# Optimization experiments

Measured on AMD Instinct MI355X. Metric: run time of the kernel, lower is better.

## Reference

```python
import jax, jax.numpy as jnp
import numpy as np
import math

D_MODEL = 1024
NUM_HEADS = 16
HEAD = D_MODEL // NUM_HEADS
EPS = 1e-5


def setup_inputs() -> dict:
    key = jax.random.key(0)
    ks = jax.random.split(key, 5)
    x = jax.random.normal(ks[0], (2, 2048, D_MODEL), dtype=jnp.float32)
    # parameters (torch.rand -> uniform [0,1) per the module; scaled here for numerics)
    wq = jax.random.uniform(ks[1], (NUM_HEADS, D_MODEL, HEAD), dtype=jnp.float32) * 0.02
    wk = jax.random.uniform(ks[2], (NUM_HEADS, D_MODEL, HEAD), dtype=jnp.float32) * 0.02
    wv = jax.random.uniform(ks[3], (NUM_HEADS, D_MODEL, HEAD), dtype=jnp.float32) * 0.02
    wo = jax.random.uniform(ks[4], (D_MODEL, D_MODEL), dtype=jnp.float32) * 0.02
    ln_w = jnp.ones((D_MODEL,), dtype=jnp.float32)
    ln_b = jnp.zeros((D_MODEL,), dtype=jnp.float32)
    return {"x": x, "ln_w": ln_w, "ln_b": ln_b, "wq": wq, "wk": wk, "wv": wv, "wo": wo}


def _layernorm(x, w, b):
    mean = jnp.mean(x, axis=-1, keepdims=True)
    var = jnp.var(x, axis=-1, keepdims=True)
    return (x - mean) * w / jnp.sqrt(var + EPS) + b


def reference(x, ln_w, ln_b, wq, wk, wv, wo):
    # pre-norm
    y = _layernorm(x, ln_w, ln_b)  # [b, s, d]
    seq_len = y.shape[-2]
    # per-head projections: [b, h, s, e]
    q = jnp.einsum('bsd,hde->bhse', y, wq)
    k = jnp.einsum('bsd,hde->bhse', y, wk)
    v = jnp.einsum('bsd,hde->bhse', y, wv)
    scores = jnp.einsum('bhse,bhte->bhst', q, k) / math.sqrt(HEAD)
    causal = jnp.triu(jnp.full((seq_len, seq_len), -jnp.inf, dtype=scores.dtype), k=1)
    scores = scores + causal
    weights = jax.nn.softmax(scores, axis=-1)
    attn = jnp.einsum('bhst,bhte->bshe', weights, v)  # merged transpose
    attn = attn.reshape(*attn.shape[:-2], -1)  # [b, s, d]
    out = attn @ wo
    return out + x
```

## Files before the change

### kernel.cpp

```cpp
#include <hip/hip_runtime.h>
#include <stdint.h>

typedef __bf16 bf16;
typedef __bf16 bf16x2 __attribute__((ext_vector_type(2)));
typedef __bf16 bf16x4 __attribute__((ext_vector_type(4)));
typedef __bf16 bf16x8 __attribute__((ext_vector_type(8)));
typedef float f32x4 __attribute__((ext_vector_type(4)));
typedef unsigned int u32;
typedef u32 u32x4 __attribute__((ext_vector_type(4)));

#define D_MODEL 1024
#define NHEADS 16
#define HEADDIM 64
#define SEQ 2048
#define NBATCH 2

__device__ __forceinline__ void async_load16(const void* g, void* l) {
  __builtin_amdgcn_global_load_lds(
      (__attribute__((address_space(1))) void*)g,
      (__attribute__((address_space(3))) void*)l, 16, 0, 0);
}

__device__ __forceinline__ float fexp2(float x) {
#if __has_builtin(__builtin_amdgcn_exp2f)
  return __builtin_amdgcn_exp2f(x);
#else
  return exp2f(x);
#endif
}

__device__ __forceinline__ void pswap32(u32& x, u32& y) {
  asm("v_permlane32_swap_b32 %0, %1" : "+v"(x), "+v"(y));
}
__device__ __forceinline__ void pswap16(u32& x, u32& y) {
  asm("v_permlane16_swap_b32 %0, %1" : "+v"(x), "+v"(y));
}

__global__ __launch_bounds__(256)
void ln_and_transpose(const float* __restrict__ x, const float* __restrict__ lw,
                      const float* __restrict__ lb, bf16* __restrict__ y,
                      const float* __restrict__ wq, const float* __restrict__ wk,
                      const float* __restrict__ wv, const float* __restrict__ wo,
                      bf16* __restrict__ WqkvT, bf16* __restrict__ woT) {
  __shared__ float tile[64][65];
  __shared__ float ps[4], pq[4];
  int t = threadIdx.x;
  if (blockIdx.x < 4096) {
    int row = blockIdx.x;
    const float4 v = ((const float4*)(x + (size_t)row * D_MODEL))[t];
    float s = v.x + v.y + v.z + v.w;
    float sq = v.x * v.x + v.y * v.y + v.z * v.z + v.w * v.w;
#pragma unroll
    for (int d = 1; d < 64; d <<= 1) {
      s += __shfl_xor(s, d);
      sq += __shfl_xor(sq, d);
    }
    if ((t & 63) == 0) { ps[t >> 6] = s; pq[t >> 6] = sq; }
    __syncthreads();
    s = ps[0] + ps[1] + ps[2] + ps[3];
    sq = pq[0] + pq[1] + pq[2] + pq[3];
    float mean = s * (1.0f / D_MODEL);
    float var = sq * (1.0f / D_MODEL) - mean * mean;
    float rstd = rsqrtf(var + 1e-5f);
    float4 wv4 = ((const float4*)lw)[t];
    float4 bv = ((const float4*)lb)[t];
    bf16x4 o;
    o[0] = (bf16)((v.x - mean) * rstd * wv4.x + bv.x);
    o[1] = (bf16)((v.y - mean) * rstd * wv4.y + bv.y);
    o[2] = (bf16)((v.z - mean) * rstd * wv4.z + bv.z);
    o[3] = (bf16)((v.w - mean) * rstd * wv4.w + bv.w);
    ((bf16x4*)(y + (size_t)row * D_MODEL))[t] = o;
    return;
  }
  int blk = blockIdx.x - 4096;
  const float* s;
  bf16* d;
  int src_ld, dst_ld;
  if (blk < 768) {
    int wsel = blk >> 8;
    int rem = blk & 255;
    int h = rem >> 4, tr = rem & 15;
    const float* w3 = (wsel == 0) ? wq : (wsel == 1) ? wk : wv;
    s = w3 + (size_t)h * 65536 + (size_t)tr * 64 * 64;
    d = WqkvT + ((size_t)wsel << 20) + (size_t)h * 65536 + (size_t)tr * 64;
    src_ld = 64; dst_ld = 1024;
  } else {
    int r = blk - 768;
    int tr = r >> 4, tc = r & 15;
    s = wo + (size_t)(tr * 64) * 1024 + tc * 64;
    d = woT + (size_t)(tc * 64) * 1024 + tr * 64;
    src_ld = 1024; dst_ld = 1024;
  }
  int rr = t >> 4;
  int cc = (t & 15) << 2;
#pragma unroll
  for (int i = 0; i < 4; ++i) {
    float4 v = *(const float4*)&s[(size_t)(rr + i * 16) * src_ld + cc];
    tile[rr + i * 16][cc + 0] = v.x;
    tile[rr + i * 16][cc + 1] = v.y;
    tile[rr + i * 16][cc + 2] = v.z;
    tile[rr + i * 16][cc + 3] = v.w;
  }
  __syncthreads();
#pragma unroll
  for (int i = 0; i < 4; ++i) {
    int drow = rr + i * 16;
    bf16x4 o;
    o[0] = (bf16)tile[cc + 0][drow];
    o[1] = (bf16)tile[cc + 1][drow];
    o[2] = (bf16)tile[cc + 2][drow];
    o[3] = (bf16)tile[cc + 3][drow];
    *(bf16x4*)&d[(size_t)drow * dst_ld + cc] = o;
  }
}

template <int MODE, int BM, int BN>
__global__ __launch_bounds__(256)
void gemm_bt(const bf16* __restrict__ A, const bf16* __restrict__ Bt,
             int ntn, void* __restrict__ p0, void* __restrict__ p1,
             void* __restrict__ p2) {
  constexpr int NWR = BM / 64;
  constexpr int NWC = 4 / NWR;
  constexpr int NJ = BN / (16 * NWC);
  __shared__ __align__(16) bf16 As[2][BM * 64];
  __shared__ __align__(16) bf16 Bs[2][BN * 64];
  int cpx = gridDim.x >> 3;
  int wg = (blockIdx.x & 7) * cpx + (blockIdx.x >> 3);
  int bm = wg / ntn;
  int bn = wg % ntn;
  int t = threadIdx.x;
  int w = t >> 6, l = t & 63;
  int lg = l >> 4, lo = l & 15;
  int wr = w / NWC, wc = w % NWC;
  const bf16* Ab = A + (size_t)bm * BM * 1024;
  const bf16* Bb = Bt + (size_t)bn * BN * 1024;
  f32x4 acc[4][NJ];
#pragma unroll
  for (int i = 0; i < 4; ++i)
#pragma unroll
    for (int j = 0; j < NJ; ++j) acc[i][j] = (f32x4){0.f, 0.f, 0.f, 0.f};

  auto stage = [&](int bufi, int k0) {
#pragma unroll
    for (int it = 0; it < BM / 32; ++it) {
      int flat = it * 2048 + t * 8;
      int row = flat >> 6, sc = ((flat & 63) >> 3) ^ (row & 7);
      async_load16(Ab + (size_t)row * 1024 + k0 + sc * 8, &As[bufi][it * 2048 + w * 512]);
    }
#pragma unroll
    for (int it = 0; it < BN / 32; ++it) {
      int flat = it * 2048 + t * 8;
      int row = flat >> 6, sc = ((flat & 63) >> 3) ^ (row & 7);
      async_load16(Bb + (size_t)row * 1024 + k0 + sc * 8, &Bs[bufi][it * 2048 + w * 512]);
    }
  };

  stage(0, 0);
  __syncthreads();
  int buf = 0;
  for (int k0 = 0; k0 < 1024; k0 += 64) {
    if (k0 + 64 < 1024) stage(buf ^ 1, k0 + 64);
#pragma unroll
    for (int kk = 0; kk < 2; ++kk) {
      bf16x8 af[4], bfr[NJ];
#pragma unroll
      for (int i = 0; i < 4; ++i) {
        int row = wr * 64 + i * 16 + lo;
        af[i] = *(const bf16x8*)&As[buf][row * 64 + (((4 * kk + lg) ^ (lo & 7)) * 8)];
      }
#pragma unroll
      for (int j = 0; j < NJ; ++j) {
        int row = wc * (NJ * 16) + j * 16 + lo;
        bfr[j] = *(const bf16x8*)&Bs[buf][row * 64 + (((4 * kk + lg) ^ (lo & 7)) * 8)];
      }
#pragma unroll
      for (int i = 0; i < 4; ++i)
#pragma unroll
        for (int j = 0; j < NJ; ++j)
          acc[i][j] = __builtin_amdgcn_mfma_f32_16x16x32_bf16(af[i], bfr[j], acc[i][j], 0, 0, 0);
    }
    __syncthreads();
    buf ^= 1;
  }

  int mbase = bm * BM + wr * 64;
  int nbase = bn * BN + wc * (NJ * 16);
#pragma unroll
  for (int i = 0; i < 4; ++i) {
#pragma unroll
    for (int j = 0; j < NJ; ++j) {
      int row0 = mbase + i * 16 + lg * 4;
      int col = nbase + j * 16 + lo;
      if (MODE == 0) {
        if (col < 2048) {
          bf16* dst = (bf16*)(col < 1024 ? p0 : p1);
          int c = col & 1023;
          int h = c >> 6, e = c & 63;
#pragma unroll
          for (int r = 0; r < 4; ++r) {
            int row = row0 + r;
            dst[((((size_t)(row >> 11) * NHEADS + h) * SEQ) + (row & 2047)) * HEADDIM + e] =
                (bf16)acc[i][j][r];
          }
        } else {
          int c = col - 2048;
          int h = c >> 6, e = c & 63;
          int b_ = row0 >> 11, s_ = row0 & 2047;
          bf16x4 pk;
          pk[0] = (bf16)acc[i][j][0]; pk[1] = (bf16)acc[i][j][1];
          pk[2] = (bf16)acc[i][j][2]; pk[3] = (bf16)acc[i][j][3];
          *(bf16x4*)&((bf16*)p2)[(((size_t)b_ * NHEADS + h) * HEADDIM + e) * SEQ + s_] = pk;
        }
      } else {
#pragma unroll
        for (int r = 0; r < 4; ++r) {
          int row = row0 + r;
          float xr = ((const float*)p1)[(size_t)row * 1024 + col];
          ((float*)p0)[(size_t)row * 1024 + col] = acc[i][j][r] + xr;
        }
      }
    }
  }
}

__global__ __launch_bounds__(512)
void attn_kernel(const bf16* __restrict__ q, const bf16* __restrict__ k,
                 const bf16* __restrict__ vt, bf16* __restrict__ attn,
                 bf16* __restrict__ pO, float* __restrict__ plsum) {
  __shared__ __align__(16) bf16 Ks[2][64 * 64];
  __shared__ __align__(16) bf16 Vs[2][64 * 64];
  const float C2 = 0.125f * 1.44269504f;
  const float MC = 128.0f * C2;
  int i = blockIdx.x;
  int slot = i >> 3;
  int bh = (i & 7) + 8 * (slot & 3);
  int ji = slot >> 2;
  int split, tb;
  if (ji < 8) { split = 0; tb = ji; }
  else { split = 1 + ((ji >> 4) & 1); tb = 15 - (ji & 7); }
  int c0 = (split == 2) ? tb + 1 : 0;
  int c1 = (split == 1) ? tb + 1 : 2 * tb + 2;
  int b = bh >> 4, h = bh & 15;
  int t = threadIdx.x, w = t >> 6, l = t & 63;
  int lg = l >> 4, lo = l & 15;
  const bf16* qp = q + (size_t)bh * SEQ * HEADDIM;
  const bf16* kp = k + (size_t)bh * SEQ * HEADDIM;
  const bf16* vp = vt + (size_t)bh * HEADDIM * SEQ;
  int q0 = tb * 128 + w * 16;
  int cd = q0 >> 6;
  int diag_rhs = (w & 3) * 16 + lo;

  bf16x8 qf0 = *(const bf16x8*)&qp[(size_t)(q0 + lo) * HEADDIM + 8 * lg];
  bf16x8 qf1 = *(const bf16x8*)&qp[(size_t)(q0 + lo) * HEADDIM + 32 + 8 * lg];

  auto stage = [&](int bufi, int kv0) {
    int row = t >> 3, c16 = t & 7;
    int sc = c16 ^ (row & 7);
    async_load16(kp + (size_t)(kv0 + row) * HEADDIM + sc * 8, &Ks[bufi][t * 8]);
    async_load16(vp + (size_t)row * SEQ + kv0 + sc * 8, &Vs[bufi][t * 8]);
  };

  f32x4 o[4];
#pragma unroll
  for (int nt = 0; nt < 4; ++nt) o[nt] = (f32x4){0.f, 0.f, 0.f, 0.f};
  float lsum = 0.f;

  int buf = 0;
  stage(0, c0 * 64);
  __syncthreads();

  for (int c = c0; c < c1; ++c) {
    if (c + 1 < c1) stage(buf ^ 1, (c + 1) * 64);

    if (c <= cd) {
      f32x4 s[4];
      __builtin_amdgcn_s_setprio(1);
#pragma unroll
      for (int nt = 0; nt < 4; ++nt) {
        s[nt] = (f32x4){0.f, 0.f, 0.f, 0.f};
        int krow = nt * 16 + lo;
        bf16x8 kf0 = *(const bf16x8*)&Ks[buf][krow * 64 + ((lg ^ (lo & 7)) * 8)];
        bf16x8 kf1 = *(const bf16x8*)&Ks[buf][krow * 64 + (((4 + lg) ^ (lo & 7)) * 8)];
        s[nt] = __builtin_amdgcn_mfma_f32_16x16x32_bf16(kf0, qf0, s[nt], 0, 0, 0);
        s[nt] = __builtin_amdgcn_mfma_f32_16x16x32_bf16(kf1, qf1, s[nt], 0, 0, 0);
      }
      __builtin_amdgcn_s_setprio(0);

      bf16x8 vf0[4], vf1[4];
#pragma unroll
      for (int nt = 0; nt < 4; ++nt) {
        int vrow = nt * 16 + lo;
        vf0[nt] = *(const bf16x8*)&Vs[buf][vrow * 64 + ((lg ^ (lo & 7)) * 8)];
        vf1[nt] = *(const bf16x8*)&Vs[buf][vrow * 64 + (((4 + lg) ^ (lo & 7)) * 8)];
      }

      if (c == cd) {
#pragma unroll
        for (int nt = 0; nt < 4; ++nt)
#pragma unroll
          for (int r = 0; r < 4; ++r)
            s[nt][r] = (16 * nt + 4 * lg + r <= diag_rhs) ? s[nt][r] : -1e30f;
      }

      u32 W[4][2];
      float psum = 0.f;
#pragma unroll
      for (int nt = 0; nt < 4; ++nt) {
        float e0 = fexp2(fmaf(s[nt][0], C2, -MC));
        float e1 = fexp2(fmaf(s[nt][1], C2, -MC));
        float e2 = fexp2(fmaf(s[nt][2], C2, -MC));
        float e3 = fexp2(fmaf(s[nt][3], C2, -MC));
        psum += (e0 + e1) + (e2 + e3);
        bf16x2 w0, w1;
        w0[0] = (bf16)e0; w0[1] = (bf16)e1;
        w1[0] = (bf16)e2; w1[1] = (bf16)e3;
        W[nt][0] = __builtin_bit_cast(u32, w0);
        W[nt][1] = __builtin_bit_cast(u32, w1);
      }
      psum += __shfl_xor(psum, 16);
      psum += __shfl_xor(psum, 32);
      lsum += psum;

      u32 t0 = W[0][0], t2 = W[1][0];
      pswap32(t0, t2); pswap16(t0, t2);
      u32 t1 = W[0][1], t3 = W[1][1];
      pswap32(t1, t3); pswap16(t1, t3);
      u32 u0 = W[2][0], u2 = W[3][0];
      pswap32(u0, u2); pswap16(u0, u2);
      u32 u1 = W[2][1], u3 = W[3][1];
      pswap32(u1, u3); pswap16(u1, u3);
      u32x4 pw0 = {t0, t1, t2, t3};
      u32x4 pw1 = {u0, u1, u2, u3};
      bf16x8 pf0 = __builtin_bit_cast(bf16x8, pw0);
      bf16x8 pf1 = __builtin_bit_cast(bf16x8, pw1);

      __builtin_amdgcn_s_setprio(1);
#pragma unroll
      for (int nt = 0; nt < 4; ++nt) {
        o[nt] = __builtin_amdgcn_mfma_f32_16x16x32_bf16(pf0, vf0[nt], o[nt], 0, 0, 0);
        o[nt] = __builtin_amdgcn_mfma_f32_16x16x32_bf16(pf1, vf1[nt], o[nt], 0, 0, 0);
      }
      __builtin_amdgcn_s_setprio(0);
    }

    __syncthreads();
    buf ^= 1;
  }

  if (split == 0) {
#pragma unroll
    for (int r = 0; r < 4; ++r) {
      float ls = __shfl(lsum, (l & 48) | (4 * lg + r));
      float inv = 1.0f / ls;
      int qrow = q0 + 4 * lg + r;
#pragma unroll
      for (int nt = 0; nt < 4; ++nt)
        attn[((size_t)b * SEQ + qrow) * D_MODEL + h * HEADDIM + nt * 16 + lo] =
            (bf16)(o[nt][r] * inv);
    }
  } else {
    int half = split - 1;
#pragma unroll
    for (int r = 0; r < 4; ++r) {
      float ls = __shfl(lsum, (l & 48) | (4 * lg + r));
      int prow = q0 - 1024 + 4 * lg + r;
      if (lo == 0) plsum[(half << 15) + (bh << 10) + prow] = ls;
      size_t base = (((size_t)half * 32 + bh) * 1024 + prow) * 64;
#pragma unroll
      for (int nt = 0; nt < 4; ++nt)
        pO[base + nt * 16 + lo] = (bf16)o[nt][r];
    }
  }
}

__global__ __launch_bounds__(256)
void merge_kernel(const bf16* __restrict__ pO, const float* __restrict__ plsum,
                  bf16* __restrict__ attn) {
  int tid = blockIdx.x * 256 + threadIdx.x;
  int bh = tid >> 13;
  int rem = tid & 8191;
  int srow = rem >> 3, q8 = rem & 7;
  int b = bh >> 4, h = bh & 15;
  float l = plsum[(bh << 10) + srow] + plsum[(1 << 15) + (bh << 10) + srow];
  float inv = 1.0f / l;
  size_t base = (((size_t)bh) * 1024 + srow) * 64 + q8 * 8;
  bf16x8 a1 = *(const bf16x8*)&pO[base];
  bf16x8 a2 = *(const bf16x8*)&pO[(size_t)32 * 1024 * 64 + base];
  bf16x8 o;
#pragma unroll
  for (int e = 0; e < 8; ++e)
    o[e] = (bf16)(((float)a1[e] + (float)a2[e]) * inv);
  *(bf16x8*)&attn[((size_t)b * SEQ + 1024 + srow) * D_MODEL + h * HEADDIM + q8 * 8] = o;
}

extern "C" void kernel_launch(void* const* d_in, const int* in_sizes, int n_in,
                              void* d_out, int out_size, void* d_ws, size_t ws_size,
                              hipStream_t stream) {
  const float* x = (const float*)d_in[0];
  const float* ln_w = (const float*)d_in[1];
  const float* ln_b = (const float*)d_in[2];
  const float* wq = (const float*)d_in[3];
  const float* wk = (const float*)d_in[4];
  const float* wv = (const float*)d_in[5];
  const float* wo = (const float*)d_in[6];
  float* out = (float*)d_out;
  char* ws = (char*)d_ws;

  bf16* y     = (bf16*)(ws);
  bf16* WqkvT = (bf16*)(ws + (8u << 20));
  bf16* woT   = (bf16*)(ws + (14u << 20));
  bf16* qb    = (bf16*)(ws + (16u << 20));
  bf16* kb    = (bf16*)(ws + (24u << 20));
  bf16* vtb   = (bf16*)(ws + (32u << 20));
  bf16* attnb = (bf16*)(ws + (40u << 20));
  bf16*  pO    = (bf16*)(ws);
  float* plsum = (float*)(ws + (8u << 20));

  ln_and_transpose<<<5120, 256, 0, stream>>>(x, ln_w, ln_b, y, wq, wk, wv, wo,
                                             WqkvT, woT);

  gemm_bt<0, 128, 192><<<512, 256, 0, stream>>>(y, WqkvT, 16, qb, kb, vtb);

  attn_kernel<<<dim3(768), 512, 0, stream>>>(qb, kb, vtb, attnb, pO, plsum);

  merge_kernel<<<1024, 256, 0, stream>>>(pO, plsum, attnb);

  gemm_bt<2, 64, 64><<<1024, 256, 0, stream>>>(attnb, woT, 16, out, (void*)x, nullptr);
}
```

Before: 99.32 us.

## Split long causal attention tiles three ways and retile output projection

The attention grid goes from 768 to 1024 blocks. Each late query tile (tb 8-15) is now split into three key ranges instead of two, and the unsplit tiles are reordered so the largest are issued first. The merge kernel combines three partial outputs and sums, and the partial-sum buffer is moved to make room for the third partition. The output projection GEMM switches to 64x128 tiles with half the blocks, and attention gets a min-blocks launch bound hint. The goal is better load balance across CUs for causal attention, at the cost of extra partial writes and merge traffic.

```diff
diff --git a/kernel.cpp b/kernel.cpp
--- a/kernel.cpp
+++ b/kernel.cpp
@@ -223,7 +223,7 @@
   }
 }
 
-__global__ __launch_bounds__(512)
+__global__ __launch_bounds__(512, 8)
 void attn_kernel(const bf16* __restrict__ q, const bf16* __restrict__ k,
                  const bf16* __restrict__ vt, bf16* __restrict__ attn,
                  bf16* __restrict__ pO, float* __restrict__ plsum) {
@@ -235,11 +235,20 @@
   int slot = i >> 3;
   int bh = (i & 7) + 8 * (slot & 3);
   int ji = slot >> 2;
-  int split, tb;
-  if (ji < 8) { split = 0; tb = ji; }
-  else { split = 1 + ((ji >> 4) & 1); tb = 15 - (ji & 7); }
-  int c0 = (split == 2) ? tb + 1 : 0;
-  int c1 = (split == 1) ? tb + 1 : 2 * tb + 2;
+  int tb, c0, c1, part;
+  bool issplit = (ji >= 8);
+  if (!issplit) {
+    tb = 7 - ji; part = 0;
+    c0 = 0; c1 = 2 * tb + 2;
+  } else {
+    int e = (ji - 8) & 7;
+    part = (ji - 8) >> 3;
+    tb = 8 + e;
+    int n = 2 * tb + 2;
+    int s0 = (n + 2) / 3, s1 = (n + 1) / 3;
+    c0 = (part == 0) ? 0 : ((part == 1) ? s0 : s0 + s1);
+    c1 = (part == 0) ? s0 : ((part == 1) ? s0 + s1 : n);
+  }
   int b = bh >> 4, h = bh & 15;
   int t = threadIdx.x, w = t >> 6, l = t & 63;
   int lg = l >> 4, lo = l & 15;
@@ -347,7 +356,7 @@
     buf ^= 1;
   }
 
-  if (split == 0) {
+  if (!issplit) {
 #pragma unroll
     for (int r = 0; r < 4; ++r) {
       float ls = __shfl(lsum, (l & 48) | (4 * lg + r));
@@ -359,13 +368,12 @@
             (bf16)(o[nt][r] * inv);
     }
   } else {
-    int half = split - 1;
 #pragma unroll
     for (int r = 0; r < 4; ++r) {
       float ls = __shfl(lsum, (l & 48) | (4 * lg + r));
       int prow = q0 - 1024 + 4 * lg + r;
-      if (lo == 0) plsum[(half << 15) + (bh << 10) + prow] = ls;
-      size_t base = (((size_t)half * 32 + bh) * 1024 + prow) * 64;
+      if (lo == 0) plsum[(part << 15) + (bh << 10) + prow] = ls;
+      size_t base = (((size_t)part * 32 + bh) * 1024 + prow) * 64;
 #pragma unroll
       for (int nt = 0; nt < 4; ++nt)
         pO[base + nt * 16 + lo] = (bf16)o[nt][r];
@@ -381,15 +389,18 @@
   int rem = tid & 8191;
   int srow = rem >> 3, q8 = rem & 7;
   int b = bh >> 4, h = bh & 15;
-  float l = plsum[(bh << 10) + srow] + plsum[(1 << 15) + (bh << 10) + srow];
-  float inv = 1.0f / l;
+  int lidx = (bh << 10) + srow;
+  float lsum = plsum[lidx] + plsum[(1 << 15) + lidx] + plsum[(2 << 15) + lidx];
+  float inv = 1.0f / lsum;
+  const size_t PSTRIDE = (size_t)32 * 1024 * 64;
   size_t base = (((size_t)bh) * 1024 + srow) * 64 + q8 * 8;
-  bf16x8 a1 = *(const bf16x8*)&pO[base];
-  bf16x8 a2 = *(const bf16x8*)&pO[(size_t)32 * 1024 * 64 + base];
+  bf16x8 a0 = *(const bf16x8*)&pO[base];
+  bf16x8 a1 = *(const bf16x8*)&pO[PSTRIDE + base];
+  bf16x8 a2 = *(const bf16x8*)&pO[2 * PSTRIDE + base];
   bf16x8 o;
 #pragma unroll
   for (int e = 0; e < 8; ++e)
-    o[e] = (bf16)(((float)a1[e] + (float)a2[e]) * inv);
+    o[e] = (bf16)((((float)a0[e] + (float)a1[e]) + (float)a2[e]) * inv);
   *(bf16x8*)&attn[((size_t)b * SEQ + 1024 + srow) * D_MODEL + h * HEADDIM + q8 * 8] = o;
 }
 
@@ -414,16 +425,16 @@
   bf16* vtb   = (bf16*)(ws + (32u << 20));
   bf16* attnb = (bf16*)(ws + (40u << 20));
   bf16*  pO    = (bf16*)(ws);
-  float* plsum = (float*)(ws + (8u << 20));
+  float* plsum = (float*)(ws + (12u << 20));
 
   ln_and_transpose<<<5120, 256, 0, stream>>>(x, ln_w, ln_b, y, wq, wk, wv, wo,
                                              WqkvT, woT);
 
   gemm_bt<0, 128, 192><<<512, 256, 0, stream>>>(y, WqkvT, 16, qb, kb, vtb);
 
-  attn_kernel<<<dim3(768), 512, 0, stream>>>(qb, kb, vtb, attnb, pO, plsum);
+  attn_kernel<<<dim3(1024), 512, 0, stream>>>(qb, kb, vtb, attnb, pO, plsum);
 
   merge_kernel<<<1024, 256, 0, stream>>>(pO, plsum, attnb);
 
-  gemm_bt<2, 64, 64><<<1024, 256, 0, stream>>>(attnb, woT, 16, out, (void*)x, nullptr);
-}
+  gemm_bt<2, 64, 128><<<512, 256, 0, stream>>>(attnb, woT, 8, out, (void*)x, nullptr);
+}
```

Result: slower. 199.8 us (+101.2%).
